# Kernel optimization log

Measured on AMD Instinct MI355X. Metric: run time of the kernel, lower is better.

Reference implementation:

```python
import jax, jax.numpy as jnp
import numpy as np

B, T, H, CH = 8192, 10, 512, 512  # batch, time_step, hidden_size, code_hidden_size (must be equal)


def setup_inputs() -> dict:
    key = jax.random.key(0)
    ks = jax.random.split(key, 18)
    s = 0.05
    inp = {
        "h": jax.random.normal(ks[0], (B, T, CH), dtype=jnp.float32),
        "y_seq": jax.random.normal(ks[1], (B, T), dtype=jnp.float32),
        "attn1_w": jax.random.normal(ks[2], (CH, 2 * H), dtype=jnp.float32) * s,
        "attn1_b": jax.random.normal(ks[3], (CH,), dtype=jnp.float32) * s,
        "attn2_w": jax.random.normal(ks[4], (CH, CH), dtype=jnp.float32) * s,
        "attn2_b": jax.random.normal(ks[5], (CH,), dtype=jnp.float32) * s,
        "attn3_w": jax.random.normal(ks[6], (1, CH), dtype=jnp.float32) * s,
        "attn3_b": jax.random.normal(ks[7], (1,), dtype=jnp.float32) * s,
        "W_ih": jax.random.normal(ks[8], (4 * H, 1), dtype=jnp.float32) * s,
        "W_hh": jax.random.normal(ks[9], (4 * H, H), dtype=jnp.float32) * s,
        "b_ih": jax.random.normal(ks[10], (4 * H,), dtype=jnp.float32) * s,
        "b_hh": jax.random.normal(ks[11], (4 * H,), dtype=jnp.float32) * s,
        "fc1_w": jax.random.normal(ks[12], (H, CH + H), dtype=jnp.float32) * s,
        "fc1_b": jax.random.normal(ks[13], (H,), dtype=jnp.float32) * s,
        "fc2_w": jax.random.normal(ks[14], (1, H), dtype=jnp.float32) * s,
        "fc2_b": jax.random.normal(ks[15], (1,), dtype=jnp.float32) * s,
    }
    return inp


def reference(h, y_seq, attn1_w, attn1_b, attn2_w, attn2_b, attn3_w, attn3_b,
              W_ih, W_hh, b_ih, b_hh, fc1_w, fc1_b, fc2_w, fc2_b):
    # h: [B, T, CH] -> scan over time; y_seq: [B, T]
    h_t = jnp.transpose(h, (1, 0, 2))      # [T, B, CH]
    y_t = jnp.transpose(y_seq, (1, 0))     # [T, B]
    b = h.shape[0]
    hid = W_hh.shape[1]
    d0 = jnp.zeros((b, hid), dtype=h.dtype)
    s0 = jnp.zeros((b, hid), dtype=h.dtype)

    def step(carry, xs):
        d, s = carry
        ht, yt = xs  # ht: [B, CH], yt: [B]
        # attention scores (note: original softmax is over a singleton dim -> weights == 1)
        x = jnp.concatenate([d, ht], axis=1)                       # [B, 2H]
        a = jnp.tanh((x @ attn1_w.T + attn1_b) @ attn2_w.T + attn2_b)
        w = a @ attn3_w.T + attn3_b                                # [B, 1]
        w = jax.nn.softmax(w, axis=1)                              # softmax over size-1 dim == 1
        h1 = w * ht                                                # [B, H] (CH == H)
        # single LSTM step with h0 = h1, c0 = s, input = yt (scalar feature)
        gates = yt[:, None] @ W_ih.T + b_ih + h1 @ W_hh.T + b_hh   # [B, 4H]
        i, f, g, o = jnp.split(gates, 4, axis=1)
        c = jax.nn.sigmoid(f) * s + jax.nn.sigmoid(i) * jnp.tanh(g)
        d_new = jax.nn.sigmoid(o) * jnp.tanh(c)
        return (d_new, c), None

    (d, s), _ = jax.lax.scan(step, (d0, s0), (h_t, y_t))
    z = jnp.concatenate([d, h_t[-1]], axis=1)                      # [B, CH+H]
    y_res = (z @ fc1_w.T + fc1_b) @ fc2_w.T + fc2_b                # [B, 1]
    return y_res
```

## Files before the change

kernel.cpp:

```cpp
#include <hip/hip_runtime.h>
#include <stdint.h>

typedef __attribute__((ext_vector_type(8))) short short8;
typedef __attribute__((ext_vector_type(4))) float f32x4;
typedef unsigned short ushort_t;

#define T_STEPS 10
#define WPACK_BYTES (2048*1024)
#define VBUF_OFF  WPACK_BYTES
#define HBF_OFF   (WPACK_BYTES + 8192)
#define H_ELEMS   (8192ull*T_STEPS*512)
#define HBF_BYTES (H_ELEMS*2)

typedef const __attribute__((address_space(1))) void gas_void;
typedef __attribute__((address_space(3))) void las_void;

__device__ __forceinline__ void gld_lds16(const void* g, void* l){
  __builtin_amdgcn_global_load_lds((gas_void*)g, (las_void*)l, 16, 0, 0);
}

__device__ __forceinline__ unsigned int pk2(float x, float y){
  unsigned int bx = __float_as_uint(x), by = __float_as_uint(y);
  bx = (bx + 0x7FFFu + ((bx>>16)&1u)) >> 16;
  by = (by + 0x7FFFu + ((by>>16)&1u)) >> 16;
  return bx | (by<<16);
}
__device__ __forceinline__ float sigf(float x){ return 1.f/(1.f + __expf(-x)); }
__device__ __forceinline__ float tanh_(float x){
  x = fminf(fmaxf(x, -15.f), 15.f);
  float e = __expf(2.f*x);
  return (e - 1.f)/(e + 1.f);
}

__global__ __launch_bounds__(256) void k_pack(const float* __restrict__ Whh,
                                              ushort_t* __restrict__ wp){
  int id  = blockIdx.x*256 + threadIdx.x;
  int row = id >> 6;
  int ko  = (id & 63) * 8;
  const float* p = Whh + row*512 + ko;
  float4 a = *(const float4*)p, b = *(const float4*)(p+4);
  uint4 v;
  v.x = pk2(a.x,a.y); v.y = pk2(a.z,a.w);
  v.z = pk2(b.x,b.y); v.w = pk2(b.z,b.w);
  int g = row >> 9, j = row & 511;
  int jb = j >> 6, jt = (j >> 4) & 3, jl = j & 15;
  int kc = ko >> 5, khi = (ko >> 3) & 3, lane = khi*16 + jl;
  int chunk = ((jb*4 + jt)*4 + g)*16 + kc;
  *(uint4*)(wp + chunk*512 + lane*8) = v;
}

__global__ __launch_bounds__(256) void k_v(const float* __restrict__ fc1w,
                                           const float* __restrict__ fc1b,
                                           const float* __restrict__ fc2w,
                                           const float* __restrict__ fc2b,
                                           float* __restrict__ vout,
                                           float* __restrict__ bias0){
  __shared__ float red[4][64];
  int tid = threadIdx.x;
  if (blockIdx.x < 16){
    int j  = blockIdx.x*64 + (tid & 63);
    int hc = tid >> 6;
    float s = 0.f;
    for (int hh = hc*128; hh < hc*128 + 128; ++hh)
      s += fc2w[hh] * fc1w[hh*1024 + j];
    red[hc][tid & 63] = s;
    __syncthreads();
    if (tid < 64)
      vout[blockIdx.x*64 + tid] = red[0][tid]+red[1][tid]+red[2][tid]+red[3][tid];
  } else {
    if (tid < 64){
      float s = 0.f;
      for (int i = 0; i < 8; ++i){ int hh = i*64 + tid; s += fc2w[hh]*fc1b[hh]; }
      for (int m = 32; m; m >>= 1) s += __shfl_xor(s, m);
      if (tid == 0) *bias0 = s + fc2b[0];
    }
  }
}

__global__ __launch_bounds__(512) void k_init(const float* __restrict__ h,
                                              const float* __restrict__ v,
                                              const float* __restrict__ bias0,
                                              float* __restrict__ out){
  int w = threadIdx.x >> 6, lane = threadIdx.x & 63;
  float b0v = *bias0;
  const float* v2 = v + 512;
  for (int r = 0; r < 8; ++r){
    int b = blockIdx.x*64 + w*8 + r;
    const float* hp = h + ((size_t)b*T_STEPS + 9)*512 + lane*8;
    float4 x0 = *(const float4*)hp, x1 = *(const float4*)(hp+4);
    const float* vp = v2 + lane*8;
    float4 w0 = *(const float4*)vp, w1 = *(const float4*)(vp+4);
    float s = x0.x*w0.x + x0.y*w0.y + x0.z*w0.z + x0.w*w0.w
            + x1.x*w1.x + x1.y*w1.y + x1.z*w1.z + x1.w*w1.w;
    for (int m = 32; m; m >>= 1) s += __shfl_xor(s, m);
    if (lane == 0) out[b] = s + b0v;
  }
}

__global__ __launch_bounds__(256) void k_prep(const float* __restrict__ h,
                                              ushort_t* __restrict__ hbf){
  __shared__ __align__(16) ushort_t buf[8192*8];
  int bid = blockIdx.x;
  int T = bid / 20, rem = bid % 20, t = rem >> 1, half = rem & 1;
  int tid = threadIdx.x;
  int row128 = tid >> 1, khalf = tid & 1;
  const float* src = h + ((size_t)(T*256 + half*128 + row128)*T_STEPS + t)*512
                   + khalf*256;
#pragma unroll
  for (int g = 0; g < 32; ++g){
    int k0 = khalf*256 + g*8;
    float4 a = *(const float4*)(src + g*8);
    float4 b = *(const float4*)(src + g*8 + 4);
    uint4 pk;
    pk.x = pk2(a.x,a.y); pk.y = pk2(a.z,a.w);
    pk.z = pk2(b.x,b.y); pk.w = pk2(b.z,b.w);
    int kc = k0 >> 5, kq = (k0 >> 3) & 3;
    *(uint4*)&buf[(size_t)(kc*512 + kq*128 + row128)*8] = pk;
  }
  __syncthreads();
  size_t sb = ((size_t)(T*T_STEPS + t)*16)*1024;
#pragma unroll
  for (int i = 0; i < 32; ++i){
    int gr = tid + i*256;
    int kc = gr >> 9, kq = (gr >> 7) & 3, r = gr & 127;
    size_t dg = sb + (size_t)kc*1024 + kq*256 + half*128 + r;
    *(uint4*)(hbf + dg*8) = *(const uint4*)&buf[gr*8];
  }
}

__global__ __launch_bounds__(512)
__attribute__((amdgpu_waves_per_eu(4)))
void k_main_p(const ushort_t* __restrict__ hbf, const float* __restrict__ y,
              const float* __restrict__ Wih, const float* __restrict__ bih,
              const float* __restrict__ bhh,
              const ushort_t* __restrict__ wpack, const float* __restrict__ v1,
              float* __restrict__ out)
{
  __shared__ __align__(16) ushort_t Wlds[48*512];
  __shared__ float ys[256*T_STEPS];

  int tid = threadIdx.x;
  int w = tid >> 6, lane = tid & 63, lhi = lane >> 4, llo = lane & 15;
  int bid = blockIdx.x;
  int xcd = bid & 7, q = bid >> 3;
  int jb  = q & 31;
  int tile = xcd*4 + (q >> 5);
  int b0 = tile * 256;

  float bias2[4], wihv[4];
#pragma unroll
  for (int g = 0; g < 4; ++g){
    int col = g*512 + jb*16 + llo;
    bias2[g] = bih[col] + bhh[col];
    wihv[g]  = Wih[col];
  }
  float v1v = v1[jb*16 + llo];

  for (int i = tid; i < 256*T_STEPS; i += 512)
    ys[i] = y[(size_t)b0*T_STEPS + i];

#pragma unroll
  for (int i = 0; i < 6; ++i){
    int c = w*6 + i;
    int g = c >> 4, kc = c & 15;
    int ch = (jb*4 + g)*16 + kc;
    gld_lds16(wpack + (size_t)ch*512 + lane*8, Wlds + c*512);
  }
  __syncthreads();

  const ushort_t* wl = Wlds + lane*8;
  const ushort_t* aT = hbf + (size_t)tile*1310720
                     + (size_t)(lhi*256 + w*32 + llo)*8;

  f32x4 acc[2][3];
  float cst[2][4];
#pragma unroll
  for (int m = 0; m < 2; ++m){
#pragma unroll
    for (int g = 0; g < 3; ++g) acc[m][g] = (f32x4){0.f,0.f,0.f,0.f};
#pragma unroll
    for (int r = 0; r < 4; ++r) cst[m][r] = 0.f;
  }

#pragma unroll 1
  for (int t = 0; t < T_STEPS; ++t){
    const ushort_t* ap = aT;
    short8 afA[2], wfA[3], afB[2], wfB[3];
#pragma unroll
    for (int m = 0; m < 2; ++m) afA[m] = *(const short8*)(ap + m*128);
#pragma unroll
    for (int g = 0; g < 3; ++g)
      wfA[g] = *(const short8*)(wl + g*8192);

#pragma unroll 1
    for (int kp = 0; kp < 8; ++kp){
      const ushort_t* wk1 = wl + (2*kp + 1)*512;
#pragma unroll
      for (int m = 0; m < 2; ++m) afB[m] = *(const short8*)(ap + 8192 + m*128);
#pragma unroll
      for (int g = 0; g < 3; ++g)
        wfB[g] = *(const short8*)(wk1 + g*8192);
#pragma unroll
      for (int g = 0; g < 3; ++g)
#pragma unroll
        for (int m = 0; m < 2; ++m)
          acc[m][g] = __builtin_amdgcn_mfma_f32_16x16x32_bf16(
              afA[m], wfA[g], acc[m][g], 0, 0, 0);
      if (kp < 7){
        const ushort_t* wk2 = wl + (2*kp + 2)*512;
#pragma unroll
        for (int m = 0; m < 2; ++m) afA[m] = *(const short8*)(ap + 16384 + m*128);
#pragma unroll
        for (int g = 0; g < 3; ++g)
          wfA[g] = *(const short8*)(wk2 + g*8192);
      }
#pragma unroll
      for (int g = 0; g < 3; ++g)
#pragma unroll
        for (int m = 0; m < 2; ++m)
          acc[m][g] = __builtin_amdgcn_mfma_f32_16x16x32_bf16(
              afB[m], wfB[g], acc[m][g], 0, 0, 0);
      ap += 16384;
    }

#pragma unroll
    for (int m = 0; m < 2; ++m)
#pragma unroll
      for (int r = 0; r < 4; ++r){
        float yr = ys[(w*32 + m*16 + lhi*4 + r)*T_STEPS + t];
        float pi = acc[m][0][r] + fmaf(yr, wihv[0], bias2[0]);
        float pf = acc[m][1][r] + fmaf(yr, wihv[1], bias2[1]);
        float pg = acc[m][2][r] + fmaf(yr, wihv[2], bias2[2]);
        cst[m][r] = sigf(pf)*cst[m][r] + sigf(pi)*tanh_(pg);
      }
#pragma unroll
    for (int m = 0; m < 2; ++m)
#pragma unroll
      for (int g = 0; g < 3; ++g) acc[m][g] = (f32x4){0.f,0.f,0.f,0.f};

    aT += 131072;
  }

  f32x4 acco[2];
#pragma unroll
  for (int m = 0; m < 2; ++m) acco[m] = (f32x4){0.f,0.f,0.f,0.f};

  {
    const ushort_t* ap = aT - 131072;
    const ushort_t* wo = wpack + (size_t)((jb*4 + 3)*16)*512 + lane*8;
    short8 afA[2], woA, afB[2], woB;
#pragma unroll
    for (int m = 0; m < 2; ++m) afA[m] = *(const short8*)(ap + m*128);
    woA = *(const short8*)(wo);

#pragma unroll 1
    for (int kp = 0; kp < 8; ++kp){
#pragma unroll
      for (int m = 0; m < 2; ++m) afB[m] = *(const short8*)(ap + 8192 + m*128);
      woB = *(const short8*)(wo + (2*kp+1)*512);
#pragma unroll
      for (int m = 0; m < 2; ++m)
        acco[m] = __builtin_amdgcn_mfma_f32_16x16x32_bf16(
            afA[m], woA, acco[m], 0, 0, 0);
      if (kp < 7){
#pragma unroll
        for (int m = 0; m < 2; ++m) afA[m] = *(const short8*)(ap + 16384 + m*128);
        woA = *(const short8*)(wo + (2*kp+2)*512);
      }
#pragma unroll
      for (int m = 0; m < 2; ++m)
        acco[m] = __builtin_amdgcn_mfma_f32_16x16x32_bf16(
            afB[m], woB, acco[m], 0, 0, 0);
      ap += 16384;
    }
  }

#pragma unroll
  for (int m = 0; m < 2; ++m)
#pragma unroll
    for (int r = 0; r < 4; ++r){
      float yr = ys[(w*32 + m*16 + lhi*4 + r)*T_STEPS + 9];
      float po = acco[m][r] + fmaf(yr, wihv[3], bias2[3]);
      float val = sigf(po)*tanh_(cst[m][r])*v1v;
      val += __shfl_xor(val, 1);
      val += __shfl_xor(val, 2);
      val += __shfl_xor(val, 4);
      val += __shfl_xor(val, 8);
      if (llo == 0)
        atomicAdd(&out[b0 + w*32 + m*16 + lhi*4 + r], val);
    }
}

__global__ __launch_bounds__(256)
__attribute__((amdgpu_waves_per_eu(2)))
void k_main_f(const float* __restrict__ h, const float* __restrict__ y,
              const float* __restrict__ Wih, const float* __restrict__ bih,
              const float* __restrict__ bhh,
              const ushort_t* __restrict__ wpack, const float* __restrict__ v1,
              float* __restrict__ out)
{
  __shared__ __align__(16) ushort_t Abf[2][4096];
  __shared__ float ysf[128*T_STEPS];

  int tid = threadIdx.x;
  int w = tid >> 6, lane = tid & 63, lhi = lane >> 4, llo = lane & 15;
  int mh = w & 1, wj = w >> 1;
  int bid = blockIdx.x;
  int xcd = bid & 7, q = bid >> 3;
  int jb = q >> 3, tile = xcd*8 + (q & 7);
  int b0 = tile * 128;

  float bias2[4][2], wihv[4][2], v1v[2];
#pragma unroll
  for (int g = 0; g < 4; ++g)
#pragma unroll
    for (int n = 0; n < 2; ++n){
      int col = g*512 + jb*64 + (wj*2+n)*16 + llo;
      bias2[g][n] = bih[col] + bhh[col];
      wihv[g][n]  = Wih[col];
    }
#pragma unroll
  for (int n = 0; n < 2; ++n) v1v[n] = v1[jb*64 + (wj*2+n)*16 + llo];

  for (int i = tid; i < 128*T_STEPS; i += 256)
    ysf[i] = y[(size_t)b0*T_STEPS + i];

  const ushort_t* wbase = wpack + (size_t)(jb*4 + wj*2)*32768 + lane*8;

  auto stageA_f = [&](int parity, int ss){
    int t = (ss < 160) ? (ss >> 4) : 9;
    int kc = ss & 15;
#pragma unroll
    for (int i = 0; i < 2; ++i){
      int gidx = tid + i*256;
      int kq = gidx >> 7, row = gidx & 127;
      const float* p = h + ((size_t)(b0+row)*T_STEPS + t)*512 + kc*32 + kq*8;
      float4 x0 = *(const float4*)p, x1 = *(const float4*)(p+4);
      uint4 pk;
      pk.x = pk2(x0.x,x0.y); pk.y = pk2(x0.z,x0.w);
      pk.z = pk2(x1.x,x1.y); pk.w = pk2(x1.z,x1.w);
      *(uint4*)&Abf[parity][gidx*8] = pk;
    }
  };

  stageA_f(0, 0);
  __syncthreads();

  f32x4 acc[4][3][2];
  float cst[4][2][4];
#pragma unroll
  for (int m = 0; m < 4; ++m)
#pragma unroll
    for (int n = 0; n < 2; ++n){
#pragma unroll
      for (int g = 0; g < 3; ++g) acc[m][g][n] = (f32x4){0.f,0.f,0.f,0.f};
#pragma unroll
      for (int r = 0; r < 4; ++r) cst[m][n][r] = 0.f;
    }

  const int aro = (lhi*128 + mh*64 + llo)*8;

#pragma unroll 1
  for (int s = 0; s < 160; ++s){
    if (s < 159) stageA_f((s+1)&1, s+1);
    else         stageA_f(0, 160);

    int kco = (s & 15) * 512;
    short8 wf[3][2];
#pragma unroll
    for (int g = 0; g < 3; ++g)
#pragma unroll
      for (int n = 0; n < 2; ++n)
        wf[g][n] = *(const short8*)(wbase + (size_t)(n*4+g)*8192 + kco);

    const ushort_t* ap = &Abf[s&1][aro];
    short8 af[4];
#pragma unroll
    for (int m = 0; m < 4; ++m)
      af[m] = *(const short8*)(ap + m*128);

#pragma unroll
    for (int g = 0; g < 3; ++g)
#pragma unroll
      for (int n = 0; n < 2; ++n)
#pragma unroll
        for (int m = 0; m < 4; ++m)
          acc[m][g][n] = __builtin_amdgcn_mfma_f32_16x16x32_bf16(
              af[m], wf[g][n], acc[m][g][n], 0, 0, 0);

    if ((s & 15) == 15){
      int t = s >> 4;
#pragma unroll
      for (int m = 0; m < 4; ++m)
#pragma unroll
        for (int r = 0; r < 4; ++r){
          float yr = ysf[(mh*64 + m*16 + lhi*4 + r)*T_STEPS + t];
#pragma unroll
          for (int n = 0; n < 2; ++n){
            float pi = acc[m][0][n][r] + fmaf(yr, wihv[0][n], bias2[0][n]);
            float pf = acc[m][1][n][r] + fmaf(yr, wihv[1][n], bias2[1][n]);
            float pg = acc[m][2][n][r] + fmaf(yr, wihv[2][n], bias2[2][n]);
            cst[m][n][r] = sigf(pf)*cst[m][n][r] + sigf(pi)*tanh_(pg);
          }
        }
#pragma unroll
      for (int m = 0; m < 4; ++m)
#pragma unroll
        for (int g = 0; g < 3; ++g)
#pragma unroll
          for (int n = 0; n < 2; ++n) acc[m][g][n] = (f32x4){0.f,0.f,0.f,0.f};
    }
    __syncthreads();
  }

  f32x4 acco[4][2];
#pragma unroll
  for (int m = 0; m < 4; ++m)
#pragma unroll
    for (int n = 0; n < 2; ++n) acco[m][n] = (f32x4){0.f,0.f,0.f,0.f};

#pragma unroll 1
  for (int s2 = 0; s2 < 16; ++s2){
    if (s2 < 15) stageA_f((s2+1)&1, 161+s2);
    int kco = s2 * 512;
    short8 wo[2];
#pragma unroll
    for (int n = 0; n < 2; ++n)
      wo[n] = *(const short8*)(wbase + (size_t)(n*4+3)*8192 + kco);

    const ushort_t* ap = &Abf[s2&1][aro];
    short8 af[4];
#pragma unroll
    for (int m = 0; m < 4; ++m)
      af[m] = *(const short8*)(ap + m*128);
#pragma unroll
    for (int n = 0; n < 2; ++n)
#pragma unroll
      for (int m = 0; m < 4; ++m)
        acco[m][n] = __builtin_amdgcn_mfma_f32_16x16x32_bf16(
            af[m], wo[n], acco[m][n], 0, 0, 0);
    __syncthreads();
  }

#pragma unroll
  for (int m = 0; m < 4; ++m)
#pragma unroll
    for (int r = 0; r < 4; ++r){
      float yr = ysf[(mh*64 + m*16 + lhi*4 + r)*T_STEPS + 9];
      float val = 0.f;
#pragma unroll
      for (int n = 0; n < 2; ++n){
        float po = acco[m][n][r] + fmaf(yr, wihv[3][n], bias2[3][n]);
        val += sigf(po)*tanh_(cst[m][n][r])*v1v[n];
      }
      val += __shfl_xor(val, 1);
      val += __shfl_xor(val, 2);
      val += __shfl_xor(val, 4);
      val += __shfl_xor(val, 8);
      if (llo == 0)
        atomicAdd(&out[b0 + mh*64 + m*16 + lhi*4 + r], val);
    }
}

extern "C" void kernel_launch(void* const* d_in, const int* in_sizes, int n_in,
                              void* d_out, int out_size, void* d_ws, size_t ws_size,
                              hipStream_t stream){
  (void)in_sizes; (void)n_in; (void)out_size;
  const float* h    = (const float*)d_in[0];
  const float* y    = (const float*)d_in[1];
  const float* Wih  = (const float*)d_in[8];
  const float* Whh  = (const float*)d_in[9];
  const float* bih  = (const float*)d_in[10];
  const float* bhh  = (const float*)d_in[11];
  const float* fc1w = (const float*)d_in[12];
  const float* fc1b = (const float*)d_in[13];
  const float* fc2w = (const float*)d_in[14];
  const float* fc2b = (const float*)d_in[15];
  float* out = (float*)d_out;

  ushort_t* wpack = (ushort_t*)d_ws;
  float* vbuf  = (float*)((char*)d_ws + VBUF_OFF);
  float* bias0 = vbuf + 1024;
  ushort_t* hbf = (ushort_t*)((char*)d_ws + HBF_OFF);
  bool prep = ws_size >= (size_t)HBF_OFF + HBF_BYTES;

  k_pack<<<512, 256, 0, stream>>>(Whh, wpack);
  k_v<<<17, 256, 0, stream>>>(fc1w, fc1b, fc2w, fc2b, vbuf, bias0);
  if (prep)
    k_prep<<<640, 256, 0, stream>>>(h, hbf);
  k_init<<<128, 512, 0, stream>>>(h, vbuf, bias0, out);
  if (prep)
    k_main_p<<<1024, 512, 0, stream>>>(hbf, y, Wih, bih, bhh, wpack, vbuf, out);
  else
    k_main_f<<<512, 256, 0, stream>>>(h, y, Wih, bih, bhh, wpack, vbuf, out);
}
```

Measured before the change: 246.9 us.

## Widen main kernel blocks to 1024 threads covering two column tiles per block

The prepared-path main kernel now launches 512 blocks of 1024 threads. Each block covers 32 hidden columns (two 16-column sub-tiles) instead of 16, with waves split between sub-tiles and batch row groups. This halves the number of blocks that stream the same batch tile of h, so more reuse of A-fragments in L2 and fewer redundant weight setups. In exchange, LDS per block doubles, occupancy hints are removed, and register pressure under the 1024-thread launch bound may cap occupancy.

Result: slower. 258.1 us (+4.5%).

```diff
diff --git a/kernel.cpp b/kernel.cpp
--- a/kernel.cpp
+++ b/kernel.cpp
@@ -128,49 +128,49 @@
   }
 }
 
-__global__ __launch_bounds__(512)
-__attribute__((amdgpu_waves_per_eu(4)))
+__global__ __launch_bounds__(1024)
 void k_main_p(const ushort_t* __restrict__ hbf, const float* __restrict__ y,
               const float* __restrict__ Wih, const float* __restrict__ bih,
               const float* __restrict__ bhh,
               const ushort_t* __restrict__ wpack, const float* __restrict__ v1,
               float* __restrict__ out)
 {
-  __shared__ __align__(16) ushort_t Wlds[48*512];
+  __shared__ __align__(16) ushort_t Wlds[96*512];
   __shared__ float ys[256*T_STEPS];
 
   int tid = threadIdx.x;
   int w = tid >> 6, lane = tid & 63, lhi = lane >> 4, llo = lane & 15;
+  int jtw = w & 1, mg = w >> 1;
   int bid = blockIdx.x;
   int xcd = bid & 7, q = bid >> 3;
-  int jb  = q & 31;
-  int tile = xcd*4 + (q >> 5);
+  int jb  = q & 15;
+  int tile = xcd*4 + (q >> 4);
   int b0 = tile * 256;
 
   float bias2[4], wihv[4];
 #pragma unroll
   for (int g = 0; g < 4; ++g){
-    int col = g*512 + jb*16 + llo;
+    int col = g*512 + jb*32 + jtw*16 + llo;
     bias2[g] = bih[col] + bhh[col];
     wihv[g]  = Wih[col];
   }
-  float v1v = v1[jb*16 + llo];
-
-  for (int i = tid; i < 256*T_STEPS; i += 512)
+  float v1v = v1[jb*32 + jtw*16 + llo];
+
+  for (int i = tid; i < 256*T_STEPS; i += 1024)
     ys[i] = y[(size_t)b0*T_STEPS + i];
 
 #pragma unroll
   for (int i = 0; i < 6; ++i){
     int c = w*6 + i;
-    int g = c >> 4, kc = c & 15;
-    int ch = (jb*4 + g)*16 + kc;
+    int g = c >> 5, jt = (c >> 4) & 1, kc = c & 15;
+    int ch = (((jb >> 1)*4 + ((jb & 1)*2 + jt))*4 + g)*16 + kc;
     gld_lds16(wpack + (size_t)ch*512 + lane*8, Wlds + c*512);
   }
   __syncthreads();
 
-  const ushort_t* wl = Wlds + lane*8;
+  const ushort_t* wlw = Wlds + jtw*8192 + lane*8;
   const ushort_t* aT = hbf + (size_t)tile*1310720
-                     + (size_t)(lhi*256 + w*32 + llo)*8;
+                     + (size_t)(lhi*256 + mg*32 + llo)*8;
 
   f32x4 acc[2][3];
   float cst[2][4];
@@ -190,16 +190,16 @@
     for (int m = 0; m < 2; ++m) afA[m] = *(const short8*)(ap + m*128);
 #pragma unroll
     for (int g = 0; g < 3; ++g)
-      wfA[g] = *(const short8*)(wl + g*8192);
+      wfA[g] = *(const short8*)(wlw + g*16384);
 
 #pragma unroll 1
     for (int kp = 0; kp < 8; ++kp){
-      const ushort_t* wk1 = wl + (2*kp + 1)*512;
+      const ushort_t* wk1 = wlw + (2*kp + 1)*512;
 #pragma unroll
       for (int m = 0; m < 2; ++m) afB[m] = *(const short8*)(ap + 8192 + m*128);
 #pragma unroll
       for (int g = 0; g < 3; ++g)
-        wfB[g] = *(const short8*)(wk1 + g*8192);
+        wfB[g] = *(const short8*)(wk1 + g*16384);
 #pragma unroll
       for (int g = 0; g < 3; ++g)
 #pragma unroll
@@ -207,12 +207,12 @@
           acc[m][g] = __builtin_amdgcn_mfma_f32_16x16x32_bf16(
               afA[m], wfA[g], acc[m][g], 0, 0, 0);
       if (kp < 7){
-        const ushort_t* wk2 = wl + (2*kp + 2)*512;
+        const ushort_t* wk2 = wlw + (2*kp + 2)*512;
 #pragma unroll
         for (int m = 0; m < 2; ++m) afA[m] = *(const short8*)(ap + 16384 + m*128);
 #pragma unroll
         for (int g = 0; g < 3; ++g)
-          wfA[g] = *(const short8*)(wk2 + g*8192);
+          wfA[g] = *(const short8*)(wk2 + g*16384);
       }
 #pragma unroll
       for (int g = 0; g < 3; ++g)
@@ -227,7 +227,7 @@
     for (int m = 0; m < 2; ++m)
 #pragma unroll
       for (int r = 0; r < 4; ++r){
-        float yr = ys[(w*32 + m*16 + lhi*4 + r)*T_STEPS + t];
+        float yr = ys[(mg*32 + m*16 + lhi*4 + r)*T_STEPS + t];
         float pi = acc[m][0][r] + fmaf(yr, wihv[0], bias2[0]);
         float pf = acc[m][1][r] + fmaf(yr, wihv[1], bias2[1]);
         float pg = acc[m][2][r] + fmaf(yr, wihv[2], bias2[2]);
@@ -247,7 +247,8 @@
 
   {
     const ushort_t* ap = aT - 131072;
-    const ushort_t* wo = wpack + (size_t)((jb*4 + 3)*16)*512 + lane*8;
+    const ushort_t* wo = wpack
+        + (size_t)((((jb >> 1)*4 + ((jb & 1)*2 + jtw))*4 + 3)*16)*512 + lane*8;
     short8 afA[2], woA, afB[2], woB;
 #pragma unroll
     for (int m = 0; m < 2; ++m) afA[m] = *(const short8*)(ap + m*128);
@@ -279,7 +280,7 @@
   for (int m = 0; m < 2; ++m)
 #pragma unroll
     for (int r = 0; r < 4; ++r){
-      float yr = ys[(w*32 + m*16 + lhi*4 + r)*T_STEPS + 9];
+      float yr = ys[(mg*32 + m*16 + lhi*4 + r)*T_STEPS + 9];
       float po = acco[m][r] + fmaf(yr, wihv[3], bias2[3]);
       float val = sigf(po)*tanh_(cst[m][r])*v1v;
       val += __shfl_xor(val, 1);
@@ -287,12 +288,11 @@
       val += __shfl_xor(val, 4);
       val += __shfl_xor(val, 8);
       if (llo == 0)
-        atomicAdd(&out[b0 + w*32 + m*16 + lhi*4 + r], val);
+        atomicAdd(&out[b0 + mg*32 + m*16 + lhi*4 + r], val);
     }
 }
 
 __global__ __launch_bounds__(256)
-__attribute__((amdgpu_waves_per_eu(2)))
 void k_main_f(const float* __restrict__ h, const float* __restrict__ y,
               const float* __restrict__ Wih, const float* __restrict__ bih,
               const float* __restrict__ bhh,
@@ -490,7 +490,7 @@
     k_prep<<<640, 256, 0, stream>>>(h, hbf);
   k_init<<<128, 512, 0, stream>>>(h, vbuf, bias0, out);
   if (prep)
-    k_main_p<<<1024, 512, 0, stream>>>(hbf, y, Wih, bih, bhh, wpack, vbuf, out);
+    k_main_p<<<512, 1024, 0, stream>>>(hbf, y, Wih, bih, bhh, wpack, vbuf, out);
   else
     k_main_f<<<512, 256, 0, stream>>>(h, y, Wih, bih, bhh, wpack, vbuf, out);
 }
```
